# Kernel tuning notes

Measured on AMD Instinct MI355X. Metric: run time of the kernel, lower is better.

## Reference

```python
import jax, jax.numpy as jnp
import numpy as np

B, L, D, H = 2, 2048, 1024, 16
DH = D // H  # per-head dim = 64


def setup_inputs() -> dict:
    key = jax.random.key(0)
    ks = jax.random.split(key, 7)
    s = 1.0 / np.sqrt(D)
    x = jax.random.normal(ks[0], (B, L, D), dtype=jnp.float32)
    Wq = jax.random.normal(ks[1], (D, D), dtype=jnp.float32) * s
    bq = jax.random.normal(ks[2], (D,), dtype=jnp.float32) * s
    Wk = jax.random.normal(ks[3], (D, D), dtype=jnp.float32) * s
    bk = jax.random.normal(ks[4], (D,), dtype=jnp.float32) * s
    Wv = jax.random.normal(ks[5], (D, D), dtype=jnp.float32) * s
    bv = jax.random.normal(ks[6], (D,), dtype=jnp.float32) * s
    # strict upper-triangular causal mask; mask==1 means position is masked (-inf)
    atten_mask = jnp.triu(jnp.ones((L, L), dtype=jnp.int32), k=1)
    return {"x": x, "atten_mask": atten_mask, "Wq": Wq, "bq": bq,
            "Wk": Wk, "bk": bk, "Wv": Wv, "bv": bv}


def reference(x, atten_mask, Wq, bq, Wk, bk, Wv, bv):
    # nn.Linear: y = x @ W^T + b
    q = x @ Wq.T + bq  # [B,L,D]
    k = x @ Wk.T + bk
    v = x @ Wv.T + bv
    # contiguous split into heads == reshape to [B,L,H,DH]
    q = q.reshape(B, L, H, DH)
    k = k.reshape(B, L, H, DH)
    v = v.reshape(B, L, H, DH)
    scale = jnp.sqrt(jnp.float32(DH))
    scores = jnp.einsum('blhd,bmhd->bhlm', q, k) / scale  # [B,H,L,L]
    # torch.where(mask == 1, -inf, scores)
    scores = jnp.where(atten_mask[None, None] == 1, -jnp.inf, scores)
    attn = jax.nn.softmax(scores, axis=-1)
    out = jnp.einsum('bhlm,bmhd->blhd', attn, v)  # [B,L,H,DH]
    return out.reshape(B, L, D)  # concat heads along channel dim
```

## Files before the change

kernel.cpp:

```cpp
#include <hip/hip_runtime.h>
#include <hip/hip_bf16.h>

#define BDIM 2
#define LSEQ 2048
#define DMODEL 1024
#define NH 16
#define DHEAD 64
#define SP 40
#define RST 68
#define CTS 136

typedef __bf16 bf16_t;
typedef __attribute__((ext_vector_type(8))) __bf16 bf16x8;
typedef __attribute__((ext_vector_type(4))) __bf16 bf16x4;
typedef __attribute__((ext_vector_type(2))) __bf16 bf16x2;
typedef __attribute__((ext_vector_type(4))) float f32x4;
typedef __attribute__((ext_vector_type(4))) int i32x4;

static __device__ __forceinline__ f32x4 mfma16(bf16x8 a, bf16x8 b, f32x4 c) {
    return __builtin_amdgcn_mfma_f32_16x16x32_bf16(a, b, c, 0, 0, 0);
}

static __device__ __forceinline__ void load_lds16(const bf16_t* g, void* l) {
    __builtin_amdgcn_global_load_lds(
        (const __attribute__((address_space(1))) void*)g,
        (__attribute__((address_space(3))) void*)l, 16, 0, 0);
}

__global__ void convert_all(
    const float* __restrict__ x,
    const float* __restrict__ Wq, const float* __restrict__ Wk, const float* __restrict__ Wv,
    const float* __restrict__ bq, const float* __restrict__ bk, const float* __restrict__ bv,
    bf16_t* __restrict__ cx,
    bf16_t* __restrict__ cWq, bf16_t* __restrict__ cWk, bf16_t* __restrict__ cWv,
    bf16_t* __restrict__ cbq, bf16_t* __restrict__ cbk, bf16_t* __restrict__ cbv,
    float SQ)
{
    const int blk = blockIdx.x;
    const float* src; bf16_t* dst; int base, cnt; float sc = 1.0f;
    if (blk < 1024)      { src = x;  dst = cx;  base = blk * 1024;          cnt = 1024; }
    else if (blk < 1280) { src = Wq; dst = cWq; base = (blk - 1024) * 1024; cnt = 1024; sc = SQ; }
    else if (blk < 1536) { src = Wk; dst = cWk; base = (blk - 1280) * 1024; cnt = 1024; }
    else if (blk < 1792) { src = Wv; dst = cWv; base = (blk - 1536) * 1024; cnt = 1024; }
    else if (blk == 1792){ src = bq; dst = cbq; base = 0; cnt = 256; sc = SQ; }
    else if (blk == 1793){ src = bk; dst = cbk; base = 0; cnt = 256; }
    else                 { src = bv; dst = cbv; base = 0; cnt = 256; }

    for (int i = base + threadIdx.x; i < base + cnt; i += 256) {
        f32x4 v = *(const f32x4*)(src + 4 * (size_t)i);
        bf16x4 o;
        o[0] = (bf16_t)(v[0] * sc); o[1] = (bf16_t)(v[1] * sc);
        o[2] = (bf16_t)(v[2] * sc); o[3] = (bf16_t)(v[3] * sc);
        *(bf16x4*)(dst + 4 * (size_t)i) = o;
    }
}

__global__ __launch_bounds__(512, 2) void qkv_gemm(
    const bf16_t* __restrict__ x,
    const bf16_t* __restrict__ W0, const bf16_t* __restrict__ W1, const bf16_t* __restrict__ W2,
    const bf16_t* __restrict__ b0, const bf16_t* __restrict__ b1, const bf16_t* __restrict__ b2,
    bf16_t* __restrict__ yq, bf16_t* __restrict__ yk, bf16_t* __restrict__ yvT)
{
    __shared__ alignas(16) bf16_t smem[81920];

    const int tid  = threadIdx.x;
    const int lane = tid & 63;
    const int w    = tid >> 6;
    const int quad = lane >> 4;
    const int n16  = lane & 15;
    const int swz  = n16 & 7;
    const int srow = lane >> 3;
    const int schnk = (lane & 7) ^ srow;

    const int s   = blockIdx.x;
    const int sem = ((s & 7) << 3) | (s >> 3);
    const int m0  = (sem >> 2) * 256;
    const int n0  = (sem & 3) * 256;
    const int z   = blockIdx.y;

    const bf16_t* W    = (z == 0) ? W0 : ((z == 1) ? W1 : W2);
    const bf16_t* bias = (z == 0) ? b0 : ((z == 1) ? b1 : b2);

    const int wm = (w >> 2) * 128;
    const int wn = (w & 3) * 64;

    const bf16_t* gA = x + (size_t)(m0 + w * 8 + srow) * DMODEL + schnk * 8;
    const bf16_t* gB = W + (size_t)(n0 + w * 8 + srow) * DMODEL + schnk * 8;

    f32x4 acc[8][4] = {};

    auto stageA = [&](int abuf, int h, int kt) {
        bf16_t* d = smem + abuf * 16384 + (h * 128 + w * 8) * 64;
        const bf16_t* src = gA + (size_t)(h * 128) * DMODEL + kt * 64;
        load_lds16(src, d);
        load_lds16(src + (size_t)64 * DMODEL, d + 64 * 64);
    };
    auto stageB = [&](int slot, int h, int kt) {
        bf16_t* d = smem + 32768 + slot * 16384 + (h * 128 + w * 8) * 64;
        const bf16_t* src = gB + (size_t)(h * 128) * DMODEL + kt * 64;
        load_lds16(src, d);
        load_lds16(src + (size_t)64 * DMODEL, d + 64 * 64);
    };

    stageA(0, 0, 0); stageA(0, 1, 0);
    stageB(0, 0, 0); stageB(0, 1, 0);
    stageB(1, 0, 1); stageB(1, 1, 1);
    asm volatile("s_waitcnt vmcnt(4)" ::: "memory");
    __builtin_amdgcn_s_barrier();

    int bs = 0;
    for (int u = 0; u < 16; ++u) {
        const int abuf = u & 1;
        const bf16_t* Ab = smem + abuf * 16384;
        const bf16_t* Bb = smem + 32768 + bs * 16384;
        const int bs2 = (bs + 2 >= 3) ? bs - 1 : bs + 2;

        bf16x8 bfr[4][2], aX[2][2], aY[2][2];

        #pragma unroll
        for (int nt = 0; nt < 4; ++nt) {
            const bf16_t* br = Bb + (wn + nt * 16 + n16) * 64;
            bfr[nt][0] = *(const bf16x8*)(br + ((quad    ) ^ swz) * 8);
            bfr[nt][1] = *(const bf16x8*)(br + ((quad + 4) ^ swz) * 8);
        }
        #pragma unroll
        for (int m2 = 0; m2 < 2; ++m2) {
            const bf16_t* ar = Ab + (wm + m2 * 16 + n16) * 64;
            aX[m2][0] = *(const bf16x8*)(ar + ((quad    ) ^ swz) * 8);
            aX[m2][1] = *(const bf16x8*)(ar + ((quad + 4) ^ swz) * 8);
        }
        if (u + 1 < 16) { stageA(abuf ^ 1, 0, u + 1); stageA(abuf ^ 1, 1, u + 1); }
        if (u + 2 < 16) { stageB(bs2, 0, u + 2);      stageB(bs2, 1, u + 2); }

        #pragma unroll
        for (int m2 = 0; m2 < 2; ++m2) {
            const bf16_t* ar = Ab + (wm + (2 + m2) * 16 + n16) * 64;
            aY[m2][0] = *(const bf16x8*)(ar + ((quad    ) ^ swz) * 8);
            aY[m2][1] = *(const bf16x8*)(ar + ((quad + 4) ^ swz) * 8);
        }
        #pragma unroll
        for (int m2 = 0; m2 < 2; ++m2)
            #pragma unroll
            for (int nt = 0; nt < 4; ++nt) {
                acc[m2][nt] = mfma16(aX[m2][0], bfr[nt][0], acc[m2][nt]);
                acc[m2][nt] = mfma16(aX[m2][1], bfr[nt][1], acc[m2][nt]);
            }

        #pragma unroll
        for (int m2 = 0; m2 < 2; ++m2) {
            const bf16_t* ar = Ab + (wm + (4 + m2) * 16 + n16) * 64;
            aX[m2][0] = *(const bf16x8*)(ar + ((quad    ) ^ swz) * 8);
            aX[m2][1] = *(const bf16x8*)(ar + ((quad + 4) ^ swz) * 8);
        }
        #pragma unroll
        for (int m2 = 0; m2 < 2; ++m2)
            #pragma unroll
            for (int nt = 0; nt < 4; ++nt) {
                acc[2 + m2][nt] = mfma16(aY[m2][0], bfr[nt][0], acc[2 + m2][nt]);
                acc[2 + m2][nt] = mfma16(aY[m2][1], bfr[nt][1], acc[2 + m2][nt]);
            }

        #pragma unroll
        for (int m2 = 0; m2 < 2; ++m2) {
            const bf16_t* ar = Ab + (wm + (6 + m2) * 16 + n16) * 64;
            aY[m2][0] = *(const bf16x8*)(ar + ((quad    ) ^ swz) * 8);
            aY[m2][1] = *(const bf16x8*)(ar + ((quad + 4) ^ swz) * 8);
        }
        #pragma unroll
        for (int m2 = 0; m2 < 2; ++m2)
            #pragma unroll
            for (int nt = 0; nt < 4; ++nt) {
                acc[4 + m2][nt] = mfma16(aX[m2][0], bfr[nt][0], acc[4 + m2][nt]);
                acc[4 + m2][nt] = mfma16(aX[m2][1], bfr[nt][1], acc[4 + m2][nt]);
            }

        #pragma unroll
        for (int m2 = 0; m2 < 2; ++m2)
            #pragma unroll
            for (int nt = 0; nt < 4; ++nt) {
                acc[6 + m2][nt] = mfma16(aY[m2][0], bfr[nt][0], acc[6 + m2][nt]);
                acc[6 + m2][nt] = mfma16(aY[m2][1], bfr[nt][1], acc[6 + m2][nt]);
            }

        if (u < 14) asm volatile("s_waitcnt vmcnt(4)" ::: "memory");
        else        asm volatile("s_waitcnt vmcnt(0)" ::: "memory");
        __builtin_amdgcn_s_barrier();
        bs = (bs + 1 == 3) ? 0 : bs + 1;
    }

    if (z < 2) {
        bf16_t* y = (z == 0) ? yq : yk;
        bf16_t* Ct = smem;
        #pragma unroll
        for (int hp = 0; hp < 2; ++hp) {
            if (((w & 3) >> 1) == hp) {
                #pragma unroll
                for (int nt = 0; nt < 4; ++nt) {
                    const int jc = (w & 1) * 64 + nt * 16 + n16;
                    const float bv = (float)bias[n0 + hp * 128 + jc];
                    #pragma unroll
                    for (int mt = 0; mt < 8; ++mt) {
                        const int rr = wm + mt * 16 + quad * 4;
                        #pragma unroll
                        for (int r = 0; r < 4; ++r)
                            Ct[(rr + r) * CTS + jc] = (bf16_t)(acc[mt][nt][r] + bv);
                    }
                }
            }
            __syncthreads();
            const int row = tid >> 1;
            const int seg = tid & 1;
            const int hh  = (n0 >> 6) + hp * 2 + seg;
            const int i   = m0 + row;
            const int bb  = i >> 11, ll = i & 2047;
            bf16_t* dst = &y[(((size_t)bb * NH + hh) * LSEQ + ll) * DHEAD];
            const bf16_t* srcr = &Ct[row * CTS + seg * 64];
            #pragma unroll
            for (int c = 0; c < 8; ++c)
                *(bf16x8*)(dst + c * 8) = *(const bf16x8*)(srcr + c * 8);
            __syncthreads();
        }
    } else {
        #pragma unroll
        for (int nt = 0; nt < 4; ++nt) {
            const int j = n0 + wn + nt * 16 + n16;
            const float bv = (float)bias[j];
            #pragma unroll
            for (int mt = 0; mt < 8; ++mt) {
                const int i0 = m0 + wm + mt * 16 + quad * 4;
                const int bb = i0 >> 11, l = i0 & 2047;
                bf16x4 pk;
                #pragma unroll
                for (int r = 0; r < 4; ++r) pk[r] = (bf16_t)(acc[mt][nt][r] + bv);
                *(bf16x4*)(&yvT[((size_t)bb * DMODEL + j) * LSEQ + l]) = pk;
            }
        }
    }
}

__global__ __launch_bounds__(256, 2) void attn_fused(
    const bf16_t* __restrict__ qp,
    const bf16_t* __restrict__ kp,
    const bf16_t* __restrict__ vtp,
    float* __restrict__ out,
    float* __restrict__ Opart,
    float* __restrict__ ml)
{
    __shared__ alignas(16) char arena[73728];
    bf16_t* KsB = (bf16_t*)(arena);
    bf16_t* VsB = (bf16_t*)(arena + 16384);
    bf16_t* PwB = (bf16_t*)(arena + 32768);
    float*  Rex = (float*) (arena + 32768);

    const int tid  = threadIdx.x;
    const int lane = tid & 63;
    const int w    = tid >> 6;
    const int quad = lane >> 4;
    const int n16  = lane & 15;
    const int lane3 = lane >> 3;
    const int lane7 = lane & 7;
    const int swz8  = (lane7 ^ lane3) * 8;
    const int swz   = n16 & 7;

    const int wq   = (w >> 1) * 64;
    const int wkv  = (w & 1) * 32;
    const int pairI = w >> 1;
    const bool isOdd = (w & 1) != 0;
    bf16_t* Pw0 = PwB + w * (2 * 64 * SP);

    const int bh  = blockIdx.x;
    const int yy  = blockIdx.y;
    const int p   = yy & 7;
    const bool isA = (yy < 8);
    const int b = bh >> 4, h = bh & 15;
    const size_t hb = (size_t)bh * (LSEQ * DHEAD);

    float l_[4];
    f32x4 oacc[4][4];

    auto zero_state = [&]() {
        #pragma unroll
        for (int g = 0; g < 4; ++g) {
            l_[g] = 0.f;
            #pragma unroll
            for (int mv = 0; mv < 4; ++mv) { f32x4 zz = {0.f,0.f,0.f,0.f}; oacc[mv][g] = zz; }
        }
    };

    auto process = [&](int qt, int t0, int ntiles, bool maskTail) {
        int iqg[4];
        bf16x8 qb[4][2];
        #pragma unroll
        for (int g = 0; g < 4; ++g) {
            iqg[g] = qt * 128 + wq + 16 * g + n16;
            const bf16_t* qq = qp + hb + (size_t)iqg[g] * DHEAD;
            qb[g][0] = *(const bf16x8*)(qq + quad * 8);
            qb[g][1] = *(const bf16x8*)(qq + 32 + quad * 8);
        }

        const bf16_t* gk = kp  + hb + (size_t)(t0 * 64 + 16 * w + lane3) * DHEAD + swz8;
        const bf16_t* gv = vtp + hb + (size_t)(16 * w + lane3) * LSEQ + t0 * 64 + swz8;

        int buf = 0;
        {
            char* lk = (char*)KsB + w * 2048;
            char* lv = (char*)VsB + w * 2048;
            load_lds16(gk,             lk);
            load_lds16(gk + 8 * DHEAD, lk + 1024);
            load_lds16(gv,             lv);
            load_lds16(gv + 8 * LSEQ,  lv + 1024);
            gk += 64 * DHEAD; gv += 64;
        }
        __syncthreads();

        for (int it = 0; it < ntiles; ++it) {
            if (it + 1 < ntiles) {
                char* lk = (char*)KsB + (buf ^ 1) * 8192 + w * 2048;
                char* lv = (char*)VsB + (buf ^ 1) * 8192 + w * 2048;
                load_lds16(gk,             lk);
                load_lds16(gk + 8 * DHEAD, lk + 1024);
                load_lds16(gv,             lv);
                load_lds16(gv + 8 * LSEQ,  lv + 1024);
                gk += 64 * DHEAD; gv += 64;
            }

            const bf16_t* kb = KsB + buf * 4096;
            f32x4 s[2][4];
            #pragma unroll
            for (int m = 0; m < 2; ++m) {
                const bf16_t* krow = kb + (wkv + 16 * m + n16) * 64;
                bf16x8 k0v = *(const bf16x8*)(krow + ((quad    ) ^ swz) * 8);
                bf16x8 k1v = *(const bf16x8*)(krow + ((quad + 4) ^ swz) * 8);
                #pragma unroll
                for (int g = 0; g < 4; ++g) {
                    f32x4 z = {0.f, 0.f, 0.f, 0.f};
                    z = mfma16(k0v, qb[g][0], z);
                    z = mfma16(k1v, qb[g][1], z);
                    s[m][g] = z;
                }
            }

            if (maskTail && it >= ntiles - 2) {
                const int k0 = (t0 + it) * 64 + wkv;
                #pragma unroll
                for (int m = 0; m < 2; ++m)
                    #pragma unroll
                    for (int g = 0; g < 4; ++g)
                        #pragma unroll
                        for (int r = 0; r < 4; ++r)
                            if (k0 + 16 * m + quad * 4 + r > iqg[g]) s[m][g][r] = -1e30f;
            }

            bf16_t* pwb = Pw0 + buf * (64 * SP);
            #pragma unroll
            for (int g = 0; g < 4; ++g) {
                float rs = 0.f;
                #pragma unroll
                for (int m = 0; m < 2; ++m) {
                    float p0 = __builtin_amdgcn_exp2f(s[m][g][0]);
                    float p1 = __builtin_amdgcn_exp2f(s[m][g][1]);
                    float p2 = __builtin_amdgcn_exp2f(s[m][g][2]);
                    float p3 = __builtin_amdgcn_exp2f(s[m][g][3]);
                    rs += (p0 + p1) + (p2 + p3);
                    bf16x4 pk;
                    pk[0] = (bf16_t)p0; pk[1] = (bf16_t)p1;
                    pk[2] = (bf16_t)p2; pk[3] = (bf16_t)p3;
                    *(bf16x4*)(pwb + (16 * g + n16) * SP + 16 * m + quad * 4) = pk;
                }
                l_[g] += rs;
            }

            asm volatile("s_waitcnt lgkmcnt(0)" ::: "memory");

            const bf16_t* vb = VsB + buf * 4096;
            bf16x8 pb[4];
            #pragma unroll
            for (int g = 0; g < 4; ++g)
                pb[g] = *(const bf16x8*)(pwb + (16 * g + n16) * SP + quad * 8);
            #pragma unroll
            for (int mv = 0; mv < 4; ++mv) {
                const bf16_t* vrow = vb + (16 * mv + n16) * 64;
                bf16x8 va = *(const bf16x8*)(vrow + ((((w & 1) * 4) + quad) ^ swz) * 8);
                #pragma unroll
                for (int g = 0; g < 4; ++g)
                    oacc[mv][g] = mfma16(va, pb[g], oacc[mv][g]);
            }

            __syncthreads();
            buf ^= 1;
        }
    };

    auto reduce_pair = [&]() {
        __syncthreads();
        float* Rb = Rex + pairI * (64 * RST);
        if (isOdd) {
            #pragma unroll
            for (int g = 0; g < 4; ++g) {
                #pragma unroll
                for (int mv = 0; mv < 4; ++mv)
                    *(f32x4*)(Rb + (16 * g + n16) * RST + 16 * mv + quad * 4) = oacc[mv][g];
                Rb[(16 * g + n16) * RST + 64 + quad] = l_[g];
            }
        }
        __syncthreads();
        if (!isOdd) {
            #pragma unroll
            for (int g = 0; g < 4; ++g) {
                #pragma unroll
                for (int mv = 0; mv < 4; ++mv) {
                    f32x4 t = *(const f32x4*)(Rb + (16 * g + n16) * RST + 16 * mv + quad * 4);
                    oacc[mv][g][0] += t[0]; oacc[mv][g][1] += t[1];
                    oacc[mv][g][2] += t[2]; oacc[mv][g][3] += t[3];
                }
                float ls = l_[g] + Rb[(16 * g + n16) * RST + 64 + quad];
                ls += __shfl_xor(ls, 16, 64);
                ls += __shfl_xor(ls, 32, 64);
                l_[g] = ls;
            }
        }
    };

    auto store_partial = [&](int pidx) {
        if (isOdd) return;
        #pragma unroll
        for (int g = 0; g < 4; ++g) {
            const int row = wq + 16 * g + n16;
            float* Ob = Opart + (size_t)pidx * (128 * 64) + row * 64;
            #pragma unroll
            for (int mv = 0; mv < 4; ++mv)
                *(f32x4*)(Ob + 16 * mv + quad * 4) = oacc[mv][g];
            if (quad == 0) ml[(size_t)pidx * 128 + row] = l_[g];
        }
    };

    if (isA) {
        zero_state();
        process(p, 0, 2 * p + 2, true);
        reduce_pair();
        if (!isOdd) {
            #pragma unroll
            for (int g = 0; g < 4; ++g) {
                const float inv = 1.0f / l_[g];
                const int iq = p * 128 + wq + 16 * g + n16;
                float* orow = out + ((size_t)b * LSEQ + iq) * DMODEL + h * DHEAD;
                #pragma unroll
                for (int mv = 0; mv < 4; ++mv) {
                    f32x4 o;
                    o[0] = oacc[mv][g][0] * inv; o[1] = oacc[mv][g][1] * inv;
                    o[2] = oacc[mv][g][2] * inv; o[3] = oacc[mv][g][3] * inv;
                    *(f32x4*)(orow + 16 * mv + quad * 4) = o;
                }
            }
        }
        zero_state();
        process(15 - p, 0, 15 - 2 * p, false);
        reduce_pair();
        store_partial((bh * 8 + (7 - p)) * 2 + 0);
    } else {
        zero_state();
        process(15 - p, 15 - 2 * p, 17, true);
        reduce_pair();
        store_partial((bh * 8 + (7 - p)) * 2 + 1);
    }
}

__global__ __launch_bounds__(256) void attn_combine(
    const float* __restrict__ Opart, const float* __restrict__ ml,
    float* __restrict__ out)
{
    const int bh = blockIdx.x;
    const int q8 = blockIdx.y;
    const int t  = threadIdx.x;
    const int row = t >> 1;
    const int dh0 = (t & 1) * 32;
    const int p0  = (bh * 8 + q8) * 2;
    const int b = bh >> 4, h = bh & 15;

    float l0 = ml[(size_t)p0 * 128 + row];
    float l1 = ml[(size_t)(p0 + 1) * 128 + row];
    float inv = 1.0f / (l0 + l1);

    const float* P0 = Opart + (size_t)p0 * (128 * 64) + row * 64 + dh0;
    const float* P1 = P0 + 128 * 64;
    float* orow = out + ((size_t)b * LSEQ + ((8 + q8) * 128 + row)) * DMODEL
                + h * DHEAD + dh0;
    #pragma unroll
    for (int c = 0; c < 8; ++c) {
        f32x4 o0 = *(const f32x4*)(P0 + 4 * c);
        f32x4 o1 = *(const f32x4*)(P1 + 4 * c);
        f32x4 o;
        o[0] = (o0[0] + o1[0]) * inv;
        o[1] = (o0[1] + o1[1]) * inv;
        o[2] = (o0[2] + o1[2]) * inv;
        o[3] = (o0[3] + o1[3]) * inv;
        *(f32x4*)(orow + 4 * c) = o;
    }
}

extern "C" void kernel_launch(void* const* d_in, const int* in_sizes, int n_in,
                              void* d_out, int out_size, void* d_ws, size_t ws_size,
                              hipStream_t stream)
{
    const float* x  = (const float*)d_in[0];
    const float* Wq = (const float*)d_in[2];
    const float* bq = (const float*)d_in[3];
    const float* Wk = (const float*)d_in[4];
    const float* bk = (const float*)d_in[5];
    const float* Wv = (const float*)d_in[6];
    const float* bv = (const float*)d_in[7];
    float* out = (float*)d_out;

    char* ws = (char*)d_ws;
    bf16_t* q   = (bf16_t*)(ws);
    bf16_t* k   = (bf16_t*)(ws + 8u  * 1024 * 1024);
    bf16_t* vT  = (bf16_t*)(ws + 16u * 1024 * 1024);
    bf16_t* cx  = (bf16_t*)(ws + 24u * 1024 * 1024);
    bf16_t* cWq = (bf16_t*)(ws + 32u * 1024 * 1024);
    bf16_t* cWk = (bf16_t*)(ws + 34u * 1024 * 1024);
    bf16_t* cWv = (bf16_t*)(ws + 36u * 1024 * 1024);
    bf16_t* cbq = (bf16_t*)(ws + 38u * 1024 * 1024);
    bf16_t* cbk = (bf16_t*)(ws + 38u * 1024 * 1024 + 4096);
    bf16_t* cbv = (bf16_t*)(ws + 38u * 1024 * 1024 + 8192);
    float*  mlp = (float*) (ws + 39u * 1024 * 1024);
    float*  Op  = (float*) (ws + 40u * 1024 * 1024);

    const float SQ = 0.125f * 1.44269504088896f;

    convert_all<<<1795, 256, 0, stream>>>(x, Wq, Wk, Wv, bq, bk, bv,
                                          cx, cWq, cWk, cWv, cbq, cbk, cbv, SQ);

    dim3 g1(64, 3, 1);
    qkv_gemm<<<g1, 512, 0, stream>>>(cx, cWq, cWk, cWv, cbq, cbk, cbv, q, k, vT);

    dim3 g2(BDIM * NH, 16, 1);
    attn_fused<<<g2, 256, 0, stream>>>(q, k, vT, out, Op, mlp);

    dim3 g3(BDIM * NH, 8, 1);
    attn_combine<<<g3, 256, 0, stream>>>(Op, mlp, out);
}
```

Measured before the change: 166.5 us.

## Triple-buffer K/V tiles with vmcnt-based waits and single P buffer

Replaces the double-buffered K/V LDS staging in the attention kernel with a three-slot ring that prefetches two tiles ahead. The full __syncthreads at the end of each iteration becomes an explicit s_waitcnt vmcnt(4) plus s_barrier, so one tile's loads can stay in flight across the barrier. The per-wave P scratch drops from double to single buffering to make LDS room, and the total arena shrinks slightly. This aims to hide more global-load latency. It costs a more fragile synchronisation scheme, which needs an extra barrier after the pair reduction because Rex now aliases the K/V region.

```diff
diff --git a/kernel.cpp b/kernel.cpp
--- a/kernel.cpp
+++ b/kernel.cpp
@@ -246,11 +246,8 @@
     float* __restrict__ Opart,
     float* __restrict__ ml)
 {
-    __shared__ alignas(16) char arena[73728];
-    bf16_t* KsB = (bf16_t*)(arena);
-    bf16_t* VsB = (bf16_t*)(arena + 16384);
-    bf16_t* PwB = (bf16_t*)(arena + 32768);
-    float*  Rex = (float*) (arena + 32768);
+    __shared__ alignas(16) char arena[69632];
+    float* Rex = (float*)(arena);
 
     const int tid  = threadIdx.x;
     const int lane = tid & 63;
@@ -266,7 +263,7 @@
     const int wkv  = (w & 1) * 32;
     const int pairI = w >> 1;
     const bool isOdd = (w & 1) != 0;
-    bf16_t* Pw0 = PwB + w * (2 * 64 * SP);
+    bf16_t* Pw0 = (bf16_t*)(arena + 49152) + w * (64 * SP);
 
     const int bh  = blockIdx.x;
     const int yy  = blockIdx.y;
@@ -298,33 +295,31 @@
             qb[g][1] = *(const bf16x8*)(qq + 32 + quad * 8);
         }
 
-        const bf16_t* gk = kp  + hb + (size_t)(t0 * 64 + 16 * w + lane3) * DHEAD + swz8;
-        const bf16_t* gv = vtp + hb + (size_t)(16 * w + lane3) * LSEQ + t0 * 64 + swz8;
-
-        int buf = 0;
-        {
-            char* lk = (char*)KsB + w * 2048;
-            char* lv = (char*)VsB + w * 2048;
-            load_lds16(gk,             lk);
-            load_lds16(gk + 8 * DHEAD, lk + 1024);
-            load_lds16(gv,             lv);
-            load_lds16(gv + 8 * LSEQ,  lv + 1024);
-            gk += 64 * DHEAD; gv += 64;
-        }
-        __syncthreads();
-
+        const bf16_t* gk0 = kp  + hb + (size_t)(t0 * 64 + 16 * w + lane3) * DHEAD + swz8;
+        const bf16_t* gv0 = vtp + hb + (size_t)(16 * w + lane3) * LSEQ + t0 * 64 + swz8;
+
+        auto stageKV = [&](int slot, int it) {
+            char* lk = arena + slot * 8192 + w * 2048;
+            char* lv = arena + 24576 + slot * 8192 + w * 2048;
+            const bf16_t* kK = gk0 + (size_t)it * 64 * DHEAD;
+            const bf16_t* vV = gv0 + (size_t)it * 64;
+            load_lds16(kK,             lk);
+            load_lds16(kK + 8 * DHEAD, lk + 1024);
+            load_lds16(vV,             lv);
+            load_lds16(vV + 8 * LSEQ,  lv + 1024);
+        };
+
+        stageKV(0, 0);
+        if (ntiles > 1) { stageKV(1, 1); asm volatile("s_waitcnt vmcnt(4)" ::: "memory"); }
+        else            {                asm volatile("s_waitcnt vmcnt(0)" ::: "memory"); }
+        __builtin_amdgcn_s_barrier();
+
+        int slot = 0;
         for (int it = 0; it < ntiles; ++it) {
-            if (it + 1 < ntiles) {
-                char* lk = (char*)KsB + (buf ^ 1) * 8192 + w * 2048;
-                char* lv = (char*)VsB + (buf ^ 1) * 8192 + w * 2048;
-                load_lds16(gk,             lk);
-                load_lds16(gk + 8 * DHEAD, lk + 1024);
-                load_lds16(gv,             lv);
-                load_lds16(gv + 8 * LSEQ,  lv + 1024);
-                gk += 64 * DHEAD; gv += 64;
-            }
-
-            const bf16_t* kb = KsB + buf * 4096;
+            const int s2 = (slot + 2 >= 3) ? slot - 1 : slot + 2;
+            if (it + 2 < ntiles) stageKV(s2, it + 2);
+
+            const bf16_t* kb = (const bf16_t*)(arena + slot * 8192);
             f32x4 s[2][4];
             #pragma unroll
             for (int m = 0; m < 2; ++m) {
@@ -351,7 +346,6 @@
                             if (k0 + 16 * m + quad * 4 + r > iqg[g]) s[m][g][r] = -1e30f;
             }
 
-            bf16_t* pwb = Pw0 + buf * (64 * SP);
             #pragma unroll
             for (int g = 0; g < 4; ++g) {
                 float rs = 0.f;
@@ -365,18 +359,18 @@
                     bf16x4 pk;
                     pk[0] = (bf16_t)p0; pk[1] = (bf16_t)p1;
                     pk[2] = (bf16_t)p2; pk[3] = (bf16_t)p3;
-                    *(bf16x4*)(pwb + (16 * g + n16) * SP + 16 * m + quad * 4) = pk;
+                    *(bf16x4*)(Pw0 + (16 * g + n16) * SP + 16 * m + quad * 4) = pk;
                 }
                 l_[g] += rs;
             }
 
             asm volatile("s_waitcnt lgkmcnt(0)" ::: "memory");
 
-            const bf16_t* vb = VsB + buf * 4096;
+            const bf16_t* vb = (const bf16_t*)(arena + 24576 + slot * 8192);
             bf16x8 pb[4];
             #pragma unroll
             for (int g = 0; g < 4; ++g)
-                pb[g] = *(const bf16x8*)(pwb + (16 * g + n16) * SP + quad * 8);
+                pb[g] = *(const bf16x8*)(Pw0 + (16 * g + n16) * SP + quad * 8);
             #pragma unroll
             for (int mv = 0; mv < 4; ++mv) {
                 const bf16_t* vrow = vb + (16 * mv + n16) * 64;
@@ -386,8 +380,10 @@
                     oacc[mv][g] = mfma16(va, pb[g], oacc[mv][g]);
             }
 
-            __syncthreads();
-            buf ^= 1;
+            if (it + 2 < ntiles) asm volatile("s_waitcnt vmcnt(4)" ::: "memory");
+            else                 asm volatile("s_waitcnt vmcnt(0)" ::: "memory");
+            __builtin_amdgcn_s_barrier();
+            slot = (slot + 1 == 3) ? 0 : slot + 1;
         }
     };
 
@@ -419,6 +415,7 @@
                 l_[g] = ls;
             }
         }
+        __syncthreads();
     };
 
     auto store_partial = [&](int pidx) {
```

After: 167.3 us (median of 2 runs). No clear change (+0.5%).
